# Optimization experiments

Hardware: AMD Instinct MI355X
Metric: run time of the kernel (lower is better)

Reference implementation:

```python
import jax, jax.numpy as jnp
import numpy as np

EPS = 1e-5

def _layernorm(x, g, b):
    mu = jnp.mean(x, axis=-1, keepdims=True)
    var = jnp.mean(jnp.square(x - mu), axis=-1, keepdims=True)
    return (x - mu) * jax.lax.rsqrt(var + EPS) * g + b

def setup_inputs() -> dict:
    key = jax.random.key(0)
    ks = jax.random.split(key, 6)
    B, S, D, F = 32768, 8, 192, 384
    sd = 1.0 / np.sqrt(D)
    return {
        "x": jax.random.normal(ks[0], (B, S, D), jnp.float32),
        "w_qkv": jax.random.normal(ks[1], (D, 3 * D), jnp.float32) * sd,
        "w_out": jax.random.normal(ks[2], (D, D), jnp.float32) * sd,
        "b_out": jnp.zeros((D,), jnp.float32),
        "g1": jnp.ones((D,), jnp.float32),
        "b1": jnp.zeros((D,), jnp.float32),
        "g2": jnp.ones((D,), jnp.float32),
        "b2": jnp.zeros((D,), jnp.float32),
        "w_f1": jax.random.normal(ks[3], (D, F), jnp.float32) * sd,
        "b_f1": jnp.zeros((F,), jnp.float32),
        "w_f2": jax.random.normal(ks[4], (F, D), jnp.float32) * (1.0 / np.sqrt(F)),
        "b_f2": jnp.zeros((D,), jnp.float32),
    }

def reference(x, w_qkv, w_out, b_out, g1, b1, g2, b2, w_f1, b_f1, w_f2, b_f2):
    B, S, D = x.shape
    H = 4
    DH = D // H
    scale = DH ** -0.5
    normed = _layernorm(x, g1, b1)
    qkv = jnp.einsum('bsd,de->bse', normed, w_qkv)  # (B,S,3D)
    q, k, v = jnp.split(qkv, 3, axis=-1)
    q = q.reshape(B, S, H, DH)
    k = k.reshape(B, S, H, DH)
    v = v.reshape(B, S, H, DH)
    attn = jnp.einsum('bqhd,bkhd->bhqk', q, k) * scale
    attn = jax.nn.softmax(attn, axis=-1)
    out = jnp.einsum('bhqk,bkhd->bqhd', attn, v).reshape(B, S, D)
    out = jnp.einsum('bsd,de->bse', out, w_out) + b_out
    x = x + out
    h = _layernorm(x, g2, b2)
    h = jax.nn.gelu(jnp.einsum('bsd,df->bsf', h, w_f1) + b_f1, approximate=False)
    h = jnp.einsum('bsf,fd->bsd', h, w_f2) + b_f2
    return x + h
```

## Files before the change

### kernel.cpp

```cpp
#include <hip/hip_runtime.h>
#include <hip/hip_bf16.h>

typedef __bf16 bf16x8 __attribute__((ext_vector_type(8)));
typedef float f32x4 __attribute__((ext_vector_type(4)));

#define DEV static __device__ __forceinline__

DEV unsigned short f2b(float f) {
  return __builtin_bit_cast(unsigned short, __float2bfloat16(f));
}
DEV unsigned pk2(float a, float b) {
  return (unsigned)f2b(a) | ((unsigned)f2b(b) << 16);
}
DEV void unpack2(unsigned u, float& lo, float& hi) {
  lo = __uint_as_float(u << 16);
  hi = __uint_as_float(u & 0xffff0000u);
}

__global__ void pack_weights(const float* __restrict__ wq,
                             const float* __restrict__ wo,
                             const float* __restrict__ wf1,
                             const float* __restrict__ wf2,
                             unsigned short* __restrict__ ws) {
  int i = blockIdx.x * 256 + threadIdx.x;
  const float* src; int j, N, KC;
  if (i < 110592)      { j = i;          src = wq;  N = 576; KC = 6; }
  else if (i < 147456) { j = i - 110592; src = wo;  N = 192; KC = 6; }
  else if (i < 221184) { j = i - 147456; src = wf1; N = 384; KC = 6; }
  else                 { j = i - 221184; src = wf2; N = 192; KC = 12; }
  int tk = j >> 9, r = j & 511;
  int nt = tk / KC, kc = tk % KC;
  int n = nt * 16 + (r >> 5), k = kc * 32 + (r & 31);
  ws[i] = f2b(src[k * N + n]);
}

template<int NT, int KC, typename EPI>
DEV void gemm_stage(const unsigned short* As, int astride,
                    const unsigned short* Bp, int nt0, int KCtot,
                    int lr, int kg, EPI epi) {
  bf16x8 af[2][KC];
  #pragma unroll
  for (int m = 0; m < 2; ++m)
    #pragma unroll
    for (int kc = 0; kc < KC; ++kc)
      af[m][kc] = *(const bf16x8*)(As + (m * 16 + lr) * astride + kc * 32 + kg * 8);
  #pragma unroll
  for (int nt = 0; nt < NT; ++nt) {
    f32x4 acc[2] = {};
    const unsigned short* bp = Bp + (size_t)((nt0 + nt) * KCtot) * 512 + lr * 32 + kg * 8;
    #pragma unroll
    for (int kc = 0; kc < KC; ++kc) {
      bf16x8 bv = *(const bf16x8*)(bp + kc * 512);
      #pragma unroll
      for (int m = 0; m < 2; ++m)
        acc[m] = __builtin_amdgcn_mfma_f32_16x16x32_bf16(bv, af[m][kc], acc[m], 0, 0, 0);
    }
    epi(nt, acc);
  }
}

DEV void layernorm_pass(const float* xm, unsigned short* dst, int dstride,
                        const float* __restrict__ gg, const float* __restrict__ bb,
                        int t) {
  int r = t >> 3, q = t & 7;
  float vals[24];
  float s = 0.f, ss = 0.f;
  #pragma unroll
  for (int j = 0; j < 6; ++j) {
    float4 v = *(const float4*)(xm + r * 196 + q * 24 + j * 4);
    vals[j*4+0] = v.x; vals[j*4+1] = v.y; vals[j*4+2] = v.z; vals[j*4+3] = v.w;
    s  += v.x + v.y + v.z + v.w;
    ss += v.x*v.x + v.y*v.y + v.z*v.z + v.w*v.w;
  }
  s  += __shfl_xor(s, 1);  s  += __shfl_xor(s, 2);  s  += __shfl_xor(s, 4);
  ss += __shfl_xor(ss, 1); ss += __shfl_xor(ss, 2); ss += __shfl_xor(ss, 4);
  float mu  = s * (1.f / 192.f);
  float var = ss * (1.f / 192.f) - mu * mu;
  float rstd = rsqrtf(var + 1e-5f);
  #pragma unroll
  for (int j = 0; j < 6; ++j) {
    int c = q * 24 + j * 4;
    float4 g4 = *(const float4*)(gg + c);
    float4 b4 = *(const float4*)(bb + c);
    uint2 u;
    u.x = pk2((vals[j*4+0] - mu) * rstd * g4.x + b4.x,
              (vals[j*4+1] - mu) * rstd * g4.y + b4.y);
    u.y = pk2((vals[j*4+2] - mu) * rstd * g4.z + b4.z,
              (vals[j*4+3] - mu) * rstd * g4.w + b4.w);
    *(uint2*)(dst + r * dstride + c) = u;
  }
}

__global__ __launch_bounds__(256, 2)
void fused_block(const float* __restrict__ x,
                 const float* __restrict__ g1, const float* __restrict__ b1,
                 const float* __restrict__ g2, const float* __restrict__ b2,
                 const float* __restrict__ b_out, const float* __restrict__ b_f1,
                 const float* __restrict__ b_f2,
                 const unsigned short* __restrict__ wq_t,
                 const unsigned short* __restrict__ wo_t,
                 const unsigned short* __restrict__ wf1_t,
                 const unsigned short* __restrict__ wf2_t,
                 float* __restrict__ out)
{
  __shared__ __align__(16) float xmid[32 * 196];
  __shared__ __align__(16) unsigned short r1[32 * 200];
  __shared__ __align__(16) unsigned short r2[18944];

  const int t = threadIdx.x;
  const int wave = t >> 6;
  const int lane = t & 63;
  const int lr = lane & 15;
  const int kg = lane >> 4;
  const int token0 = blockIdx.x * 32;

  #pragma unroll
  for (int it = 0; it < 6; ++it) {
    int idx = t + it * 256;
    int r = idx / 48, c = (idx % 48) * 4;
    *(float4*)(xmid + r * 196 + c) = *(const float4*)(x + (size_t)(token0 + r) * 192 + c);
  }
  __syncthreads();

  layernorm_pass(xmid, r1, 200, g1, b1, t);
  __syncthreads();

  gemm_stage<9, 6>(r1, 200, wq_t, wave * 9, 6, lr, kg,
    [&](int nt, f32x4 (&acc)[2]) {
      int n0 = (wave * 9 + nt) * 16 + kg * 4;
      #pragma unroll
      for (int m = 0; m < 2; ++m) {
        uint2 u; u.x = pk2(acc[m][0], acc[m][1]); u.y = pk2(acc[m][2], acc[m][3]);
        *(uint2*)(r2 + (m * 16 + lr) * 584 + n0) = u;
      }
    });
  __syncthreads();

  {
    const int g = t >> 4;
    const int qi = (t >> 1) & 7;
    const int half = t & 1;
    const int bl = g >> 2, h = g & 3;
    const int qrow = bl * 8 + qi;
    const int d0 = half * 24;
    float qv[24];
    {
      const uint4* qp = (const uint4*)(r2 + qrow * 584 + h * 48 + d0);
      #pragma unroll
      for (int u = 0; u < 3; ++u) {
        uint4 w4 = qp[u];
        unpack2(w4.x, qv[u*8+0], qv[u*8+1]);
        unpack2(w4.y, qv[u*8+2], qv[u*8+3]);
        unpack2(w4.z, qv[u*8+4], qv[u*8+5]);
        unpack2(w4.w, qv[u*8+6], qv[u*8+7]);
      }
    }
    float sc[8];
    #pragma unroll
    for (int j = 0; j < 8; ++j) {
      const uint4* kp = (const uint4*)(r2 + (bl * 8 + j) * 584 + 192 + h * 48 + d0);
      float d = 0.f;
      #pragma unroll
      for (int u = 0; u < 3; ++u) {
        uint4 w4 = kp[u];
        float lo, hi;
        unpack2(w4.x, lo, hi); d = fmaf(lo, qv[u*8+0], d); d = fmaf(hi, qv[u*8+1], d);
        unpack2(w4.y, lo, hi); d = fmaf(lo, qv[u*8+2], d); d = fmaf(hi, qv[u*8+3], d);
        unpack2(w4.z, lo, hi); d = fmaf(lo, qv[u*8+4], d); d = fmaf(hi, qv[u*8+5], d);
        unpack2(w4.w, lo, hi); d = fmaf(lo, qv[u*8+6], d); d = fmaf(hi, qv[u*8+7], d);
      }
      d += __shfl_xor(d, 1);
      sc[j] = d * 0.14433756729740643f;
    }
    float mx = sc[0];
    #pragma unroll
    for (int j = 1; j < 8; ++j) mx = fmaxf(mx, sc[j]);
    float sum = 0.f;
    #pragma unroll
    for (int j = 0; j < 8; ++j) { sc[j] = __expf(sc[j] - mx); sum += sc[j]; }
    float inv = 1.f / sum;
    float oa[24];
    #pragma unroll
    for (int e = 0; e < 24; ++e) oa[e] = 0.f;
    #pragma unroll
    for (int j = 0; j < 8; ++j) {
      float p = sc[j] * inv;
      const uint4* vp = (const uint4*)(r2 + (bl * 8 + j) * 584 + 384 + h * 48 + d0);
      #pragma unroll
      for (int u = 0; u < 3; ++u) {
        uint4 w4 = vp[u];
        float lo, hi;
        unpack2(w4.x, lo, hi); oa[u*8+0] = fmaf(p, lo, oa[u*8+0]); oa[u*8+1] = fmaf(p, hi, oa[u*8+1]);
        unpack2(w4.y, lo, hi); oa[u*8+2] = fmaf(p, lo, oa[u*8+2]); oa[u*8+3] = fmaf(p, hi, oa[u*8+3]);
        unpack2(w4.z, lo, hi); oa[u*8+4] = fmaf(p, lo, oa[u*8+4]); oa[u*8+5] = fmaf(p, hi, oa[u*8+5]);
        unpack2(w4.w, lo, hi); oa[u*8+6] = fmaf(p, lo, oa[u*8+6]); oa[u*8+7] = fmaf(p, hi, oa[u*8+7]);
      }
    }
    uint4 ov[3];
    #pragma unroll
    for (int u = 0; u < 3; ++u) {
      ov[u].x = pk2(oa[u*8+0], oa[u*8+1]);
      ov[u].y = pk2(oa[u*8+2], oa[u*8+3]);
      ov[u].z = pk2(oa[u*8+4], oa[u*8+5]);
      ov[u].w = pk2(oa[u*8+6], oa[u*8+7]);
    }
    uint4* op = (uint4*)(r1 + qrow * 200 + h * 48 + d0);
    #pragma unroll
    for (int u = 0; u < 3; ++u) op[u] = ov[u];
  }
  __syncthreads();

  gemm_stage<3, 6>(r1, 200, wo_t, wave * 3, 6, lr, kg,
    [&](int nt, f32x4 (&acc)[2]) {
      int n0 = (wave * 3 + nt) * 16 + kg * 4;
      float4 bo = *(const float4*)(b_out + n0);
      #pragma unroll
      for (int m = 0; m < 2; ++m) {
        float4* p = (float4*)(xmid + (m * 16 + lr) * 196 + n0);
        float4 v = *p;
        v.x += acc[m][0] + bo.x; v.y += acc[m][1] + bo.y;
        v.z += acc[m][2] + bo.z; v.w += acc[m][3] + bo.w;
        *p = v;
      }
    });
  __syncthreads();

  layernorm_pass(xmid, r2, 200, g2, b2, t);
  __syncthreads();

  gemm_stage<6, 6>(r2, 200, wf1_t, wave * 6, 6, lr, kg,
    [&](int nt, f32x4 (&acc)[2]) {
      int n0 = (wave * 6 + nt) * 16 + kg * 4;
      float4 bf = *(const float4*)(b_f1 + n0);
      #pragma unroll
      for (int m = 0; m < 2; ++m) {
        float ge[4];
        #pragma unroll
        for (int i = 0; i < 4; ++i) {
          float hv = acc[m][i] + ((const float*)&bf)[i];
          ge[i] = 0.5f * hv * (1.f + erff(hv * 0.70710678118654752f));
        }
        uint2 u; u.x = pk2(ge[0], ge[1]); u.y = pk2(ge[2], ge[3]);
        *(uint2*)(r2 + 6400 + (m * 16 + lr) * 392 + n0) = u;
      }
    });
  __syncthreads();

  {
    f32x4 acc[3][2] = {};
    #pragma unroll
    for (int pass = 0; pass < 2; ++pass) {
      bf16x8 af[2][6];
      #pragma unroll
      for (int m = 0; m < 2; ++m)
        #pragma unroll
        for (int kc = 0; kc < 6; ++kc)
          af[m][kc] = *(const bf16x8*)(r2 + 6400 + (m * 16 + lr) * 392 + pass * 192 + kc * 32 + kg * 8);
      #pragma unroll
      for (int nt = 0; nt < 3; ++nt) {
        const unsigned short* bp = wf2_t + (size_t)((wave * 3 + nt) * 12 + pass * 6) * 512 + lr * 32 + kg * 8;
        #pragma unroll
        for (int kc = 0; kc < 6; ++kc) {
          bf16x8 bv = *(const bf16x8*)(bp + kc * 512);
          #pragma unroll
          for (int m = 0; m < 2; ++m)
            acc[nt][m] = __builtin_amdgcn_mfma_f32_16x16x32_bf16(bv, af[m][kc], acc[nt][m], 0, 0, 0);
        }
      }
    }
    #pragma unroll
    for (int nt = 0; nt < 3; ++nt) {
      int n0 = (wave * 3 + nt) * 16 + kg * 4;
      float4 bf = *(const float4*)(b_f2 + n0);
      #pragma unroll
      for (int m = 0; m < 2; ++m) {
        float4* p = (float4*)(xmid + (m * 16 + lr) * 196 + n0);
        float4 v = *p;
        v.x += acc[nt][m][0] + bf.x; v.y += acc[nt][m][1] + bf.y;
        v.z += acc[nt][m][2] + bf.z; v.w += acc[nt][m][3] + bf.w;
        *p = v;
      }
    }
  }
  __syncthreads();

  #pragma unroll
  for (int it = 0; it < 6; ++it) {
    int idx = t + it * 256;
    int r = idx / 48, c = (idx % 48) * 4;
    *(float4*)(out + (size_t)(token0 + r) * 192 + c) = *(const float4*)(xmid + r * 196 + c);
  }
}

extern "C" void kernel_launch(void* const* d_in, const int* in_sizes, int n_in,
                              void* d_out, int out_size, void* d_ws, size_t ws_size,
                              hipStream_t stream) {
  const float* x   = (const float*)d_in[0];
  const float* wq  = (const float*)d_in[1];
  const float* wo  = (const float*)d_in[2];
  const float* bo  = (const float*)d_in[3];
  const float* g1  = (const float*)d_in[4];
  const float* b1  = (const float*)d_in[5];
  const float* g2  = (const float*)d_in[6];
  const float* b2  = (const float*)d_in[7];
  const float* wf1 = (const float*)d_in[8];
  const float* bf1 = (const float*)d_in[9];
  const float* wf2 = (const float*)d_in[10];
  const float* bf2 = (const float*)d_in[11];
  unsigned short* wsb = (unsigned short*)d_ws;

  pack_weights<<<1152, 256, 0, stream>>>(wq, wo, wf1, wf2, wsb);

  int tokens = in_sizes[0] / 192;
  int nb = tokens / 32;
  fused_block<<<nb, 256, 0, stream>>>(x, g1, b1, g2, b2, bo, bf1, bf2,
      wsb, wsb + 110592, wsb + 147456, wsb + 221184, (float*)d_out);
}
```

Baseline: 432.6 us.

## Shrink LDS footprint, drop fp32 residual buffer, split QKV GEMM, prefetch weights

Removes the fp32 xmid shared buffer by re-reading x from global memory for both layernorms and the final residual, and keeps the attention output projection as bf16 in LDS. The QKV GEMM is split into QK then V phases so the staging buffer shrinks to 392 columns, which lowers LDS use enough to raise launch bounds from 2 to 3 blocks per CU. Weight fragments are double-buffered in registers in the GEMM stages, and the FFN2 loop is restructured to prefetch A and B per k-chunk. The trade-offs are that the residual is now held at bf16 precision, global reads of x are repeated, an extra barrier is added, and register pressure may rise under the tighter launch bound.

```diff
diff --git a/kernel.cpp b/kernel.cpp
--- a/kernel.cpp
+++ b/kernel.cpp
@@ -44,39 +44,56 @@
     #pragma unroll
     for (int kc = 0; kc < KC; ++kc)
       af[m][kc] = *(const bf16x8*)(As + (m * 16 + lr) * astride + kc * 32 + kg * 8);
+  const unsigned short* bb = Bp + lr * 32 + kg * 8;
+  bf16x8 bbuf[2][KC];
+  #pragma unroll
+  for (int kc = 0; kc < KC; ++kc)
+    bbuf[0][kc] = *(const bf16x8*)(bb + (size_t)(nt0 * KCtot + kc) * 512);
   #pragma unroll
   for (int nt = 0; nt < NT; ++nt) {
+    if (nt + 1 < NT) {
+      #pragma unroll
+      for (int kc = 0; kc < KC; ++kc)
+        bbuf[(nt + 1) & 1][kc] =
+            *(const bf16x8*)(bb + (size_t)((nt0 + nt + 1) * KCtot + kc) * 512);
+    }
     f32x4 acc[2] = {};
-    const unsigned short* bp = Bp + (size_t)((nt0 + nt) * KCtot) * 512 + lr * 32 + kg * 8;
-    #pragma unroll
-    for (int kc = 0; kc < KC; ++kc) {
-      bf16x8 bv = *(const bf16x8*)(bp + kc * 512);
+    #pragma unroll
+    for (int kc = 0; kc < KC; ++kc)
       #pragma unroll
       for (int m = 0; m < 2; ++m)
-        acc[m] = __builtin_amdgcn_mfma_f32_16x16x32_bf16(bv, af[m][kc], acc[m], 0, 0, 0);
-    }
+        acc[m] = __builtin_amdgcn_mfma_f32_16x16x32_bf16(bbuf[nt & 1][kc], af[m][kc], acc[m], 0, 0, 0);
     epi(nt, acc);
   }
 }
 
-DEV void layernorm_pass(const float* xm, unsigned short* dst, int dstride,
+template<bool ADD_A>
+DEV void layernorm_pass(const float* __restrict__ xg, const unsigned short* Abuf,
+                        unsigned short* dst,
                         const float* __restrict__ gg, const float* __restrict__ bb,
                         int t) {
   int r = t >> 3, q = t & 7;
   float vals[24];
-  float s = 0.f, ss = 0.f;
+  float s = 0.f;
   #pragma unroll
   for (int j = 0; j < 6; ++j) {
-    float4 v = *(const float4*)(xm + r * 196 + q * 24 + j * 4);
+    float4 v = *(const float4*)(xg + (size_t)r * 192 + q * 24 + j * 4);
+    if (ADD_A) {
+      uint2 a2 = *(const uint2*)(Abuf + r * 200 + q * 24 + j * 4);
+      float a0, a1, a2f, a3;
+      unpack2(a2.x, a0, a1); unpack2(a2.y, a2f, a3);
+      v.x += a0; v.y += a1; v.z += a2f; v.w += a3;
+    }
     vals[j*4+0] = v.x; vals[j*4+1] = v.y; vals[j*4+2] = v.z; vals[j*4+3] = v.w;
-    s  += v.x + v.y + v.z + v.w;
-    ss += v.x*v.x + v.y*v.y + v.z*v.z + v.w*v.w;
-  }
-  s  += __shfl_xor(s, 1);  s  += __shfl_xor(s, 2);  s  += __shfl_xor(s, 4);
+    s += v.x + v.y + v.z + v.w;
+  }
+  s += __shfl_xor(s, 1); s += __shfl_xor(s, 2); s += __shfl_xor(s, 4);
+  float mu = s * (1.f / 192.f);
+  float ss = 0.f;
+  #pragma unroll
+  for (int i = 0; i < 24; ++i) { float d = vals[i] - mu; ss += d * d; }
   ss += __shfl_xor(ss, 1); ss += __shfl_xor(ss, 2); ss += __shfl_xor(ss, 4);
-  float mu  = s * (1.f / 192.f);
-  float var = ss * (1.f / 192.f) - mu * mu;
-  float rstd = rsqrtf(var + 1e-5f);
+  float rstd = rsqrtf(ss * (1.f / 192.f) + 1e-5f);
   #pragma unroll
   for (int j = 0; j < 6; ++j) {
     int c = q * 24 + j * 4;
@@ -87,11 +104,11 @@
               (vals[j*4+1] - mu) * rstd * g4.y + b4.y);
     u.y = pk2((vals[j*4+2] - mu) * rstd * g4.z + b4.z,
               (vals[j*4+3] - mu) * rstd * g4.w + b4.w);
-    *(uint2*)(dst + r * dstride + c) = u;
-  }
-}
-
-__global__ __launch_bounds__(256, 2)
+    *(uint2*)(dst + r * 200 + c) = u;
+  }
+}
+
+__global__ __launch_bounds__(256, 3)
 void fused_block(const float* __restrict__ x,
                  const float* __restrict__ g1, const float* __restrict__ b1,
                  const float* __restrict__ g2, const float* __restrict__ b2,
@@ -103,9 +120,9 @@
                  const unsigned short* __restrict__ wf2_t,
                  float* __restrict__ out)
 {
-  __shared__ __align__(16) float xmid[32 * 196];
   __shared__ __align__(16) unsigned short r1[32 * 200];
-  __shared__ __align__(16) unsigned short r2[18944];
+  __shared__ __align__(16) unsigned short bufA[32 * 200];
+  __shared__ __align__(16) unsigned short r2[32 * 392];
 
   const int t = threadIdx.x;
   const int wave = t >> 6;
@@ -113,52 +130,42 @@
   const int lr = lane & 15;
   const int kg = lane >> 4;
   const int token0 = blockIdx.x * 32;
-
-  #pragma unroll
-  for (int it = 0; it < 6; ++it) {
-    int idx = t + it * 256;
-    int r = idx / 48, c = (idx % 48) * 4;
-    *(float4*)(xmid + r * 196 + c) = *(const float4*)(x + (size_t)(token0 + r) * 192 + c);
-  }
-  __syncthreads();
-
-  layernorm_pass(xmid, r1, 200, g1, b1, t);
-  __syncthreads();
-
-  gemm_stage<9, 6>(r1, 200, wq_t, wave * 9, 6, lr, kg,
+  const float* xg = x + (size_t)token0 * 192;
+  float* og = out + (size_t)token0 * 192;
+
+  layernorm_pass<false>(xg, nullptr, r1, g1, b1, t);
+  __syncthreads();
+
+  gemm_stage<6, 6>(r1, 200, wq_t, wave * 6, 6, lr, kg,
     [&](int nt, f32x4 (&acc)[2]) {
-      int n0 = (wave * 9 + nt) * 16 + kg * 4;
+      int n0 = (wave * 6 + nt) * 16 + kg * 4;
       #pragma unroll
       for (int m = 0; m < 2; ++m) {
         uint2 u; u.x = pk2(acc[m][0], acc[m][1]); u.y = pk2(acc[m][2], acc[m][3]);
-        *(uint2*)(r2 + (m * 16 + lr) * 584 + n0) = u;
+        *(uint2*)(r2 + (m * 16 + lr) * 392 + n0) = u;
       }
     });
   __syncthreads();
 
+  const int ag = t >> 4, aqi = (t >> 1) & 7, ahalf = t & 1;
+  const int abl = ag >> 2, ah = ag & 3;
+  const int aqrow = abl * 8 + aqi;
+  const int ad0 = ahalf * 24;
+  float p[8];
   {
-    const int g = t >> 4;
-    const int qi = (t >> 1) & 7;
-    const int half = t & 1;
-    const int bl = g >> 2, h = g & 3;
-    const int qrow = bl * 8 + qi;
-    const int d0 = half * 24;
     float qv[24];
-    {
-      const uint4* qp = (const uint4*)(r2 + qrow * 584 + h * 48 + d0);
-      #pragma unroll
-      for (int u = 0; u < 3; ++u) {
-        uint4 w4 = qp[u];
-        unpack2(w4.x, qv[u*8+0], qv[u*8+1]);
-        unpack2(w4.y, qv[u*8+2], qv[u*8+3]);
-        unpack2(w4.z, qv[u*8+4], qv[u*8+5]);
-        unpack2(w4.w, qv[u*8+6], qv[u*8+7]);
-      }
-    }
-    float sc[8];
+    const uint4* qp = (const uint4*)(r2 + aqrow * 392 + ah * 48 + ad0);
+    #pragma unroll
+    for (int u = 0; u < 3; ++u) {
+      uint4 w4 = qp[u];
+      unpack2(w4.x, qv[u*8+0], qv[u*8+1]);
+      unpack2(w4.y, qv[u*8+2], qv[u*8+3]);
+      unpack2(w4.z, qv[u*8+4], qv[u*8+5]);
+      unpack2(w4.w, qv[u*8+6], qv[u*8+7]);
+    }
     #pragma unroll
     for (int j = 0; j < 8; ++j) {
-      const uint4* kp = (const uint4*)(r2 + (bl * 8 + j) * 584 + 192 + h * 48 + d0);
+      const uint4* kp = (const uint4*)(r2 + (abl * 8 + j) * 392 + 192 + ah * 48 + ad0);
       float d = 0.f;
       #pragma unroll
       for (int u = 0; u < 3; ++u) {
@@ -170,30 +177,47 @@
         unpack2(w4.w, lo, hi); d = fmaf(lo, qv[u*8+6], d); d = fmaf(hi, qv[u*8+7], d);
       }
       d += __shfl_xor(d, 1);
-      sc[j] = d * 0.14433756729740643f;
-    }
-    float mx = sc[0];
-    #pragma unroll
-    for (int j = 1; j < 8; ++j) mx = fmaxf(mx, sc[j]);
+      p[j] = d * 0.14433756729740643f;
+    }
+    float mx = p[0];
+    #pragma unroll
+    for (int j = 1; j < 8; ++j) mx = fmaxf(mx, p[j]);
     float sum = 0.f;
     #pragma unroll
-    for (int j = 0; j < 8; ++j) { sc[j] = __expf(sc[j] - mx); sum += sc[j]; }
+    for (int j = 0; j < 8; ++j) { p[j] = __expf(p[j] - mx); sum += p[j]; }
     float inv = 1.f / sum;
+    #pragma unroll
+    for (int j = 0; j < 8; ++j) p[j] *= inv;
+  }
+  __syncthreads();
+
+  gemm_stage<3, 6>(r1, 200, wq_t, 24 + wave * 3, 6, lr, kg,
+    [&](int nt, f32x4 (&acc)[2]) {
+      int n0 = (wave * 3 + nt) * 16 + kg * 4;
+      #pragma unroll
+      for (int m = 0; m < 2; ++m) {
+        uint2 u; u.x = pk2(acc[m][0], acc[m][1]); u.y = pk2(acc[m][2], acc[m][3]);
+        *(uint2*)(r2 + (m * 16 + lr) * 392 + n0) = u;
+      }
+    });
+  __syncthreads();
+
+  {
     float oa[24];
     #pragma unroll
     for (int e = 0; e < 24; ++e) oa[e] = 0.f;
     #pragma unroll
     for (int j = 0; j < 8; ++j) {
-      float p = sc[j] * inv;
-      const uint4* vp = (const uint4*)(r2 + (bl * 8 + j) * 584 + 384 + h * 48 + d0);
+      float pj = p[j];
+      const uint4* vp = (const uint4*)(r2 + (abl * 8 + j) * 392 + ah * 48 + ad0);
       #pragma unroll
       for (int u = 0; u < 3; ++u) {
         uint4 w4 = vp[u];
         float lo, hi;
-        unpack2(w4.x, lo, hi); oa[u*8+0] = fmaf(p, lo, oa[u*8+0]); oa[u*8+1] = fmaf(p, hi, oa[u*8+1]);
-        unpack2(w4.y, lo, hi); oa[u*8+2] = fmaf(p, lo, oa[u*8+2]); oa[u*8+3] = fmaf(p, hi, oa[u*8+3]);
-        unpack2(w4.z, lo, hi); oa[u*8+4] = fmaf(p, lo, oa[u*8+4]); oa[u*8+5] = fmaf(p, hi, oa[u*8+5]);
-        unpack2(w4.w, lo, hi); oa[u*8+6] = fmaf(p, lo, oa[u*8+6]); oa[u*8+7] = fmaf(p, hi, oa[u*8+7]);
+        unpack2(w4.x, lo, hi); oa[u*8+0] = fmaf(pj, lo, oa[u*8+0]); oa[u*8+1] = fmaf(pj, hi, oa[u*8+1]);
+        unpack2(w4.y, lo, hi); oa[u*8+2] = fmaf(pj, lo, oa[u*8+2]); oa[u*8+3] = fmaf(pj, hi, oa[u*8+3]);
+        unpack2(w4.z, lo, hi); oa[u*8+4] = fmaf(pj, lo, oa[u*8+4]); oa[u*8+5] = fmaf(pj, hi, oa[u*8+5]);
+        unpack2(w4.w, lo, hi); oa[u*8+6] = fmaf(pj, lo, oa[u*8+6]); oa[u*8+7] = fmaf(pj, hi, oa[u*8+7]);
       }
     }
     uint4 ov[3];
@@ -204,7 +228,7 @@
       ov[u].z = pk2(oa[u*8+4], oa[u*8+5]);
       ov[u].w = pk2(oa[u*8+6], oa[u*8+7]);
     }
-    uint4* op = (uint4*)(r1 + qrow * 200 + h * 48 + d0);
+    uint4* op = (uint4*)(r1 + aqrow * 200 + ah * 48 + ad0);
     #pragma unroll
     for (int u = 0; u < 3; ++u) op[u] = ov[u];
   }
@@ -216,19 +240,18 @@
       float4 bo = *(const float4*)(b_out + n0);
       #pragma unroll
       for (int m = 0; m < 2; ++m) {
-        float4* p = (float4*)(xmid + (m * 16 + lr) * 196 + n0);
-        float4 v = *p;
-        v.x += acc[m][0] + bo.x; v.y += acc[m][1] + bo.y;
-        v.z += acc[m][2] + bo.z; v.w += acc[m][3] + bo.w;
-        *p = v;
+        uint2 u;
+        u.x = pk2(acc[m][0] + bo.x, acc[m][1] + bo.y);
+        u.y = pk2(acc[m][2] + bo.z, acc[m][3] + bo.w);
+        *(uint2*)(bufA + (m * 16 + lr) * 200 + n0) = u;
       }
     });
   __syncthreads();
 
-  layernorm_pass(xmid, r2, 200, g2, b2, t);
-  __syncthreads();
-
-  gemm_stage<6, 6>(r2, 200, wf1_t, wave * 6, 6, lr, kg,
+  layernorm_pass<true>(xg, bufA, r1, g2, b2, t);
+  __syncthreads();
+
+  gemm_stage<6, 6>(r1, 200, wf1_t, wave * 6, 6, lr, kg,
     [&](int nt, f32x4 (&acc)[2]) {
       int n0 = (wave * 6 + nt) * 16 + kg * 4;
       float4 bf = *(const float4*)(b_f1 + n0);
@@ -241,32 +264,37 @@
           ge[i] = 0.5f * hv * (1.f + erff(hv * 0.70710678118654752f));
         }
         uint2 u; u.x = pk2(ge[0], ge[1]); u.y = pk2(ge[2], ge[3]);
-        *(uint2*)(r2 + 6400 + (m * 16 + lr) * 392 + n0) = u;
+        *(uint2*)(r2 + (m * 16 + lr) * 392 + n0) = u;
       }
     });
   __syncthreads();
 
   {
     f32x4 acc[3][2] = {};
-    #pragma unroll
-    for (int pass = 0; pass < 2; ++pass) {
-      bf16x8 af[2][6];
-      #pragma unroll
-      for (int m = 0; m < 2; ++m)
+    bf16x8 afb[2][2], bvb[2][3];
+    #pragma unroll
+    for (int m = 0; m < 2; ++m)
+      afb[0][m] = *(const bf16x8*)(r2 + (m * 16 + lr) * 392 + kg * 8);
+    #pragma unroll
+    for (int nt = 0; nt < 3; ++nt)
+      bvb[0][nt] = *(const bf16x8*)(wf2_t + (size_t)((wave * 3 + nt) * 12) * 512 + lr * 32 + kg * 8);
+    #pragma unroll
+    for (int kc = 0; kc < 12; ++kc) {
+      if (kc + 1 < 12) {
         #pragma unroll
-        for (int kc = 0; kc < 6; ++kc)
-          af[m][kc] = *(const bf16x8*)(r2 + 6400 + (m * 16 + lr) * 392 + pass * 192 + kc * 32 + kg * 8);
-      #pragma unroll
-      for (int nt = 0; nt < 3; ++nt) {
-        const unsigned short* bp = wf2_t + (size_t)((wave * 3 + nt) * 12 + pass * 6) * 512 + lr * 32 + kg * 8;
+        for (int m = 0; m < 2; ++m)
+          afb[(kc + 1) & 1][m] =
+              *(const bf16x8*)(r2 + (m * 16 + lr) * 392 + (kc + 1) * 32 + kg * 8);
         #pragma unroll
-        for (int kc = 0; kc < 6; ++kc) {
-          bf16x8 bv = *(const bf16x8*)(bp + kc * 512);
-          #pragma unroll
-          for (int m = 0; m < 2; ++m)
-            acc[nt][m] = __builtin_amdgcn_mfma_f32_16x16x32_bf16(bv, af[m][kc], acc[nt][m], 0, 0, 0);
-        }
-      }
+        for (int nt = 0; nt < 3; ++nt)
+          bvb[(kc + 1) & 1][nt] =
+              *(const bf16x8*)(wf2_t + (size_t)((wave * 3 + nt) * 12 + kc + 1) * 512 + lr * 32 + kg * 8);
+      }
+      #pragma unroll
+      for (int nt = 0; nt < 3; ++nt)
+        #pragma unroll
+        for (int m = 0; m < 2; ++m)
+          acc[nt][m] = __builtin_amdgcn_mfma_f32_16x16x32_bf16(bvb[kc & 1][nt], afb[kc & 1][m], acc[nt][m], 0, 0, 0);
     }
     #pragma unroll
     for (int nt = 0; nt < 3; ++nt) {
@@ -274,21 +302,19 @@
       float4 bf = *(const float4*)(b_f2 + n0);
       #pragma unroll
       for (int m = 0; m < 2; ++m) {
-        float4* p = (float4*)(xmid + (m * 16 + lr) * 196 + n0);
-        float4 v = *p;
-        v.x += acc[nt][m][0] + bf.x; v.y += acc[nt][m][1] + bf.y;
-        v.z += acc[nt][m][2] + bf.z; v.w += acc[nt][m][3] + bf.w;
-        *p = v;
-      }
-    }
-  }
-  __syncthreads();
-
-  #pragma unroll
-  for (int it = 0; it < 6; ++it) {
-    int idx = t + it * 256;
-    int r = idx / 48, c = (idx % 48) * 4;
-    *(float4*)(out + (size_t)(token0 + r) * 192 + c) = *(const float4*)(xmid + r * 196 + c);
+        int row = m * 16 + lr;
+        float4 xv = *(const float4*)(xg + (size_t)row * 192 + n0);
+        uint2 a2 = *(const uint2*)(bufA + row * 200 + n0);
+        float a0, a1, a2f, a3;
+        unpack2(a2.x, a0, a1); unpack2(a2.y, a2f, a3);
+        float4 o;
+        o.x = xv.x + a0  + acc[nt][m][0] + bf.x;
+        o.y = xv.y + a1  + acc[nt][m][1] + bf.y;
+        o.z = xv.z + a2f + acc[nt][m][2] + bf.z;
+        o.w = xv.w + a3  + acc[nt][m][3] + bf.w;
+        *(float4*)(og + (size_t)row * 192 + n0) = o;
+      }
+    }
   }
 }
 
```

After: 394.4 us. 1.1x faster.
